# Kernel tuning notes

Hardware: AMD Instinct MI355X
Metric: run time of the kernel (lower is better)

The kernel has to match this reference:

```python
import jax, jax.numpy as jnp
import numpy as np

PS, R, FS, SS = 3, 2, 3, 10.0
PAD = (PS - 1) // 2  # 1


def extract_patches(x, ps, stride):
    # x: (C, Hp, Wp) already padded -> (C, ps, ps, ho, wo)
    C, Hp, Wp = x.shape
    ho = (Hp - ps) // stride + 1
    wo = (Wp - ps) // stride + 1
    rows = []
    for i in range(ps):
        cols = []
        for j in range(ps):
            cols.append(x[:, i:i + stride * ho:stride, j:j + stride * wo:stride])
        rows.append(jnp.stack(cols, axis=1))
    return jnp.stack(rows, axis=1)


def fuse_diag(S):
    # conv2d of (L,L) 'image' with eye(3) kernel, zero pad 1:
    # out[u,v] = S[u-1,v-1] + S[u,v] + S[u+1,v+1]
    Sp = jnp.pad(S, 1)
    return Sp[:-2, :-2] + Sp[1:-1, 1:-1] + Sp[2:, 2:]


def ca_single(f, b, mask):
    # f, b: (c, h, w); mask: (1, h, w)
    c, h, w = f.shape
    # full-res background patches (replicate pad, stride R) -> reconstruction bank
    b_pad = jnp.pad(b, ((0, 0), (PAD, PAD), (PAD, PAD)), mode='edge')
    bg = extract_patches(b_pad, PS, R)                 # (c,ps,ps,hr,wr)
    hr, wr = bg.shape[3], bg.shape[4]
    L = hr * wr
    bg = bg.reshape(c, PS, PS, L).transpose(3, 0, 1, 2)  # (L,c,ps,ps)
    # nearest 1/R downsample (F.interpolate nearest == strided pick)
    fl = f[:, ::R, ::R]
    bl = b[:, ::R, ::R]
    ml = mask[:, ::R, ::R]
    # shrunk background patches (replicate pad, stride 1) -> matching bank
    bl_pad = jnp.pad(bl, ((0, 0), (PAD, PAD), (PAD, PAD)), mode='edge')
    bgs = extract_patches(bl_pad, PS, 1).reshape(c, PS, PS, L).transpose(3, 0, 1, 2)
    # mask patches (zero pad), valid iff patch mean == 0
    mp = extract_patches(jnp.pad(ml, ((0, 0), (PAD, PAD), (PAD, PAD))), PS, 1)
    mi = (mp.mean(axis=(1, 2)).reshape(L) == 0.0).astype(f.dtype)  # (L,)
    # L2-normalize matching patches (clamped at 1e-4)
    bnorm = jnp.maximum(jnp.sqrt((bgs ** 2).sum(axis=(1, 2, 3))), 1e-4)
    bgs_n = bgs / bnorm[:, None, None, None]
    # score = conv2d(f, patches) with zero pad 1 -> cosine-like correlation
    fp = extract_patches(jnp.pad(fl, ((0, 0), (PAD, PAD), (PAD, PAD))), PS, 1)
    score = jnp.einsum('cijhw,lcij->lhw', fp, bgs_n)   # (L,hr,wr)
    # two-pass diagonal 'fuse' trick
    S = fuse_diag(score.reshape(L, L))
    S = S.reshape(hr, wr, hr, wr).transpose(1, 0, 3, 2).reshape(L, L)
    S = fuse_diag(S)
    score = S.reshape(wr, hr, wr, hr).transpose(1, 0, 3, 2).reshape(L, hr, wr)
    # masked softmax over the L patch axis
    score = score * mi[:, None, None]
    score = jax.nn.softmax(score * SS, axis=0) * mi[:, None, None]
    # conv_transpose2d(score, bg, stride=R, padding=PAD) / 4
    # == conv of R-dilated score with flipped kernel, pad = PS-1-PAD
    w_flip = bg[:, :, ::-1, ::-1].transpose(1, 0, 2, 3)  # (c,L,ps,ps)
    out = jax.lax.conv_general_dilated(
        score[None], w_flip, window_strides=(1, 1),
        padding=[(PS - 1 - PAD, PS - 1 - PAD)] * 2, lhs_dilation=(R, R),
        dimension_numbers=('NCHW', 'OIHW', 'NCHW'))[0] / 4.0  # (c,2hr-1,2wr-1)
    if out.shape[1] % 2 == 1:  # static shape check, matches torch branch
        out = jnp.pad(out, ((0, 0), (0, 1), (0, 1)), mode='edge')
    return out


def setup_inputs() -> dict:
    key = jax.random.key(0)
    k1, k2, k3 = jax.random.split(key, 3)
    B, c, h, w = 4, 128, 128, 128
    f = jax.random.normal(k1, (B, c, h, w), dtype=jnp.float32)
    b = jax.random.normal(k2, (B, c, h, w), dtype=jnp.float32)
    mask = jax.random.bernoulli(k3, 0.25, (B, 1, h, w)).astype(jnp.float32)
    return {'f': f, 'b': b, 'mask': mask}


def reference(f, b, mask):
    return jax.vmap(ca_single)(f, b, mask)
```

## Files before the change

### kernel.cpp

```cpp
#include <hip/hip_runtime.h>
#include <cstdint>

#define LVAL 4096
#define K1 1152
#define NT1 18
#define CCH 128
#define HH 128
#define WW 128
#define SSCALE 10.0f
#define NUPAD 2048
#define NACTPAD 512
#define PADPIX 4356
#define PIMG 557568

typedef __attribute__((ext_vector_type(8))) short short8;
typedef __attribute__((ext_vector_type(8))) _Float16 half8;
typedef __attribute__((ext_vector_type(4))) float f32x4;

static __device__ __forceinline__ int clampi(int v, int lo, int hi) {
    return v < lo ? lo : (v > hi ? hi : v);
}
static __device__ __forceinline__ unsigned short f2h(float x) {
    union { _Float16 h; unsigned short u; } c; c.h = (_Float16)x; return c.u;
}
static __device__ __forceinline__ float h2f(unsigned short u) {
    union { _Float16 h; unsigned short u; } c; c.u = u; return (float)c.h;
}

__global__ __launch_bounds__(256) void dst_kernel(const float* __restrict__ f,
        const float* __restrict__ b, unsigned short* __restrict__ fpad4,
        unsigned short* __restrict__ bpad4) {
    __shared__ float t[32][65];
    int h = blockIdx.x;
    int cg = blockIdx.y;
    int za = blockIdx.z;
    int img = za >> 1, arr = za & 1;
    const float* src = (arr ? b : f) + (size_t)img * CCH * HH * WW;
    unsigned short* dst = (arr ? bpad4 : fpad4) + (size_t)img * PIMG;
    int tid = threadIdx.x;
    int w = tid & 63, csub = tid >> 6;
    #pragma unroll
    for (int cc = 0; cc < 8; ++cc) {
        int cl = csub * 8 + cc;
        int ch = cg * 32 + cl;
        t[cl][w] = src[(size_t)ch * (HH * WW) + (2 * h) * WW + (2 * w)];
    }
    __syncthreads();
    int c = tid & 31, pr = tid >> 5;
    #pragma unroll
    for (int pp = 0; pp < 8; ++pp) {
        int w2 = pr * 8 + pp;
        dst[((size_t)(h + 1) * 66 + (w2 + 1)) * 128 + cg * 32 + c] = f2h(t[c][w2]);
    }
}

__global__ __launch_bounds__(256) void qk_border_kernel(unsigned short* __restrict__ fpad4,
        unsigned short* __restrict__ bpad4, float* __restrict__ Q) {
    int img = blockIdx.y;
    int tid = threadIdx.x;
    if (blockIdx.x < 1024) {
        int lane = tid & 63, sub = tid >> 6;
        int pix = blockIdx.x * 4 + sub;
        const unsigned short* row = bpad4 + (size_t)img * PIMG
                                    + ((size_t)((pix >> 6) + 1) * 66 + (pix & 63) + 1) * 128;
        uint32_t hv = *(const uint32_t*)(row + lane * 2);
        float a = h2f((unsigned short)(hv & 0xffff));
        float b2 = h2f((unsigned short)(hv >> 16));
        float s = a * a + b2 * b2;
        for (int off = 32; off > 0; off >>= 1) s += __shfl_xor(s, off, 64);
        if (lane == 0) Q[img * 4096 + pix] = s;
    } else {
        int id = (blockIdx.x - 1024) * 256 + tid;
        if (id >= PADPIX * 16) return;
        int pix = id >> 4, cg = (id & 15) << 3;
        int hp = pix / 66, wp = pix - hp * 66;
        if (hp >= 1 && hp <= 64 && wp >= 1 && wp <= 64) return;
        unsigned short* fp = fpad4 + (size_t)img * PIMG + (size_t)pix * 128 + cg;
        #pragma unroll
        for (int cc = 0; cc < 8; ++cc) fp[cc] = 0;
        int hs = clampi(hp - 1, 0, 63), wsx = clampi(wp - 1, 0, 63);
        const unsigned short* sb = bpad4 + (size_t)img * PIMG
                                   + ((size_t)(hs + 1) * 66 + (wsx + 1)) * 128 + cg;
        unsigned short* bp = bpad4 + (size_t)img * PIMG + (size_t)pix * 128 + cg;
        #pragma unroll
        for (int cc = 0; cc < 8; ++cc) bp[cc] = sb[cc];
    }
}

__global__ __launch_bounds__(1024) void compact_kernel(const float* __restrict__ mask,
        const float* __restrict__ Q, int* __restrict__ act, int* __restrict__ ulist,
        short* __restrict__ tapu, float* __restrict__ invn, int* __restrict__ hdr) {
    int img = blockIdx.x;
    const float* mk = mask + (size_t)img * HH * WW;
    const float* Qi = Q + img * 4096;
    int* acti = act + img * NACTPAD;
    int* uli = ulist + img * NUPAD;
    short* tpi = tapu + (size_t)img * NACTPAD * 12;
    float* invi = invn + (size_t)img * NUPAD;
    int* hd = hdr + img * 4;
    int tid = threadIdx.x;
    int lane = tid & 63, wv = tid >> 6;
    __shared__ unsigned char flag[4096];
    __shared__ short umap[4096];
    __shared__ int actl[NACTPAD];
    __shared__ float ssl[4096];
    __shared__ int wsum[16], woff[16];
    __shared__ int tot;

    int loc[4];
    int cnt = 0;
    #pragma unroll
    for (int k = 0; k < 4; ++k) {
        int a = tid * 4 + k;
        int hb = a >> 6, wb = a & 63;
        float s = 0.f;
        for (int di = -1; di <= 1; ++di)
            for (int dj = -1; dj <= 1; ++dj) {
                int hh = hb + di, w2 = wb + dj;
                if (hh >= 0 && hh < 64 && w2 >= 0 && w2 < 64)
                    s += mk[(2 * hh) * WW + 2 * w2];
            }
        loc[k] = (s == 0.f) ? 1 : 0;
        cnt += loc[k];
    }
    int pre = cnt;
    for (int off = 1; off < 64; off <<= 1) { int v = __shfl_up(pre, off, 64); if (lane >= off) pre += v; }
    if (lane == 63) wsum[wv] = pre;
    __syncthreads();
    if (tid == 0) { int a2 = 0; for (int w2 = 0; w2 < 16; ++w2) { woff[w2] = a2; a2 += wsum[w2]; } tot = a2; }
    __syncthreads();
    int base = woff[wv] + pre - cnt;
    int n_act = tot < NACTPAD ? tot : NACTPAD;
    {
        int p = base;
        #pragma unroll
        for (int k = 0; k < 4; ++k)
            if (loc[k]) { if (p < NACTPAD) { acti[p] = tid * 4 + k; actl[p] = tid * 4 + k; } p++; }
    }
    #pragma unroll
    for (int k = 0; k < 4; ++k) { flag[tid * 4 + k] = 0; umap[tid * 4 + k] = -1; }
    __syncthreads();
    for (int j = tid; j < n_act; j += 1024) {
        int a = actl[j];
        int sa = ((a & 63) << 6) + (a >> 6);
        #pragma unroll
        for (int ei = 0; ei < 3; ++ei) {
            int tbt = sa + ei - 1;
            if (tbt < 0 || tbt >= 4096) continue;
            int tb = ((tbt & 63) << 6) + (tbt >> 6);
            #pragma unroll
            for (int d = -1; d <= 1; ++d) {
                int rb = tb + d;
                if (rb >= 0 && rb < 4096) flag[rb] = 1;
            }
        }
    }
    __syncthreads();
    int cnt2 = 0;
    int loc2[4];
    #pragma unroll
    for (int k = 0; k < 4; ++k) { loc2[k] = flag[tid * 4 + k]; cnt2 += loc2[k]; }
    int pre2 = cnt2;
    for (int off = 1; off < 64; off <<= 1) { int v = __shfl_up(pre2, off, 64); if (lane >= off) pre2 += v; }
    if (lane == 63) wsum[wv] = pre2;
    __syncthreads();
    if (tid == 0) { int a2 = 0; for (int w2 = 0; w2 < 16; ++w2) { woff[w2] = a2; a2 += wsum[w2]; } tot = a2; }
    __syncthreads();
    int base2 = woff[wv] + pre2 - cnt2;
    int n_u = tot < NUPAD ? tot : NUPAD;
    {
        int p = base2;
        #pragma unroll
        for (int k = 0; k < 4; ++k)
            if (loc2[k]) { int ci = tid * 4 + k; if (p < NUPAD) { uli[p] = ci; umap[ci] = (short)p; } p++; }
    }
    __syncthreads();
    for (int j = tid; j < n_act; j += 1024) {
        int a = actl[j];
        int sa = ((a & 63) << 6) + (a >> 6);
        #pragma unroll
        for (int ei = 0; ei < 3; ++ei) {
            int tbt = sa + ei - 1;
            int ok = (tbt >= 0 && tbt < 4096);
            int tb = ok ? ((tbt & 63) << 6) + (tbt >> 6) : 0;
            #pragma unroll
            for (int d = -1; d <= 1; ++d) {
                short v = -1;
                if (ok) { int rb = tb + d; if (rb >= 0 && rb < 4096) v = umap[rb]; }
                tpi[j * 12 + ei * 3 + d + 1] = v;
            }
        }
    }
    for (int a = tid; a < 4096; a += 1024) {
        int hb = a >> 6, wb = a & 63;
        float s = 0.f;
        #pragma unroll
        for (int i = 0; i < 3; ++i)
            #pragma unroll
            for (int j2 = 0; j2 < 3; ++j2) {
                int hl = clampi(hb + i - 1, 0, 63);
                int wl = clampi(wb + j2 - 1, 0, 63);
                s += Qi[hl * 64 + wl];
            }
        ssl[a] = s;
    }
    for (int u = tid; u < NUPAD; u += 1024) invi[u] = 0.f;
    __syncthreads();
    for (int ci = tid; ci < 4096; ci += 1024) {
        if (flag[ci]) {
            int u = umap[ci];
            if (u >= 0) invi[u] = 1.f / fmaxf(sqrtf(ssl[ci]), 1e-4f);
        }
    }
    if (tid == 0) { hd[0] = n_act; hd[1] = n_u; }
}

__global__ void prep_bgtc_kernel(const float* __restrict__ b, const int* __restrict__ act,
                                 const int* __restrict__ hdr, unsigned short* __restrict__ BGTc4) {
    int gimg = blockIdx.y;
    const float* bi = b + (size_t)gimg * CCH * HH * WW;
    int idx = blockIdx.x * 256 + threadIdx.x;
    int k2 = idx >> 9, j = idx & 511;
    int n_act = hdr[gimg * 4];
    unsigned short v = 0;
    if (j < n_act) {
        int a = act[gimg * NACTPAD + j];
        int ch = k2 & 127, q = k2 >> 7;
        int i = q / 3, jj = q - i * 3;
        int y = clampi(2 * (a >> 6) + i - 1, 0, 127);
        int x = clampi(2 * (a & 63) + jj - 1, 0, 127);
        v = f2h(bi[(size_t)ch * (HH * WW) + y * WW + x]);
    }
    BGTc4[(size_t)gimg * K1 * NACTPAD + idx] = v;
}

#define BAR() __builtin_amdgcn_s_barrier()
#define WAITV6() asm volatile("s_waitcnt vmcnt(6)" ::: "memory")
#define WAITV0() asm volatile("s_waitcnt vmcnt(0)" ::: "memory")

#define STAGEX(tt, h) do {                                                              \
    int t_ = (tt);                                                                      \
    if (t_ < NT1) {                                                                     \
        const int isB_ = ((h) == 1 || (h) == 2);                                        \
        const int hi_ = ((h) >= 2) ? 1 : 0;                                             \
        int q_ = t_ >> 1;                                                               \
        int qi_ = (q_ * 11) >> 5;                                                       \
        int qj_ = q_ - qi_ * 3;                                                         \
        int toff_ = ((qi_ * 66 + qj_) << 7) + ((t_ & 1) << 6);                          \
        _Pragma("unroll")                                                               \
        for (int r_ = 0; r_ < 2; ++r_) {                                                \
            int sl_ = hi_ * 2 + r_;                                                     \
            const unsigned short* g_ = (isB_ ? bR[sl_] : aR[sl_]) + toff_;              \
            unsigned short* l_ = lds + (isB_ ? 32768 : 0) + ((t_ & 1) << 14)            \
                                 + ((hi_ * 128 + r_ * 64 + swb) << 6);                  \
            __builtin_amdgcn_global_load_lds((const uint32_t*)(const void*)g_,          \
                                             (uint32_t*)(void*)l_, 16, 0, 0);           \
        }                                                                               \
    } } while (0)

#define LDA4(dst, cur, ah) do {                                                         \
    _Pragma("unroll")                                                                   \
    for (int f_ = 0; f_ < 4; ++f_)                                                      \
    { _Pragma("unroll")                                                                 \
      for (int s_ = 0; s_ < 2; ++s_) {                                                  \
        int row_ = wm * 128 + ((ah) * 4 + f_) * 16 + row16;                             \
        int cs_ = ((s_ << 2) + kgrp) ^ (row16 & 7);                                     \
        dst[f_ * 2 + s_] = *(const half8*)(lds + ((cur) << 14) + (row_ << 6) + (cs_ << 3)); \
    } } } while (0)

#define LDB2(cur, bh) do {                                                              \
    _Pragma("unroll")                                                                   \
    for (int f_ = 0; f_ < 2; ++f_)                                                      \
    { _Pragma("unroll")                                                                 \
      for (int s_ = 0; s_ < 2; ++s_) {                                                  \
        int row_ = wn * 64 + ((bh) * 2 + f_) * 16 + row16;                              \
        int cs_ = ((s_ << 2) + kgrp) ^ (row16 & 7);                                     \
        bv[(bh) * 4 + f_ * 2 + s_] = *(const half8*)(lds + 32768 + ((cur) << 14) + (row_ << 6) + (cs_ << 3)); \
    } } } while (0)

#define MFMA16(va, ai, bj) do {                                                         \
    __builtin_amdgcn_s_setprio(1);                                                      \
    _Pragma("unroll")                                                                   \
    for (int f_ = 0; f_ < 4; ++f_)                                                      \
    { _Pragma("unroll")                                                                 \
      for (int g_ = 0; g_ < 2; ++g_)                                                    \
      { _Pragma("unroll")                                                               \
        for (int s_ = 0; s_ < 2; ++s_)                                                  \
            acc[(ai) * 4 + f_][(bj) * 2 + g_] = __builtin_amdgcn_mfma_f32_16x16x32_f16( \
                va[f_ * 2 + s_], bv[(bj) * 4 + g_ * 2 + s_], acc[(ai) * 4 + f_][(bj) * 2 + g_], 0, 0, 0); \
    } } __builtin_amdgcn_s_setprio(0); } while (0)

__global__ __launch_bounds__(512, 2) void gemm1_8phase(const unsigned short* __restrict__ fpad4,
        const unsigned short* __restrict__ bpad4, unsigned short* __restrict__ Scc4,
        const int* __restrict__ ulist, const int* __restrict__ hdr,
        const float* __restrict__ invn) {
    __shared__ unsigned short lds[65536];
    const int gimg = blockIdx.y;
    const unsigned short* fpadI = fpad4 + (size_t)gimg * PIMG;
    const unsigned short* bpadI = bpad4 + (size_t)gimg * PIMG;
    unsigned short* C = Scc4 + (size_t)gimg * 4096 * NUPAD;
    const int* uli = ulist + gimg * NUPAD;
    const float* invi = invn + (size_t)gimg * NUPAD;
    const int n_u = hdr[gimg * 4 + 1];
    const int tid = threadIdx.x;
    const int lane = tid & 63;
    const int wave = tid >> 6;
    const int wm = wave >> 2, wn = wave & 3;
    const int row16 = lane & 15, kgrp = lane >> 4;
    const int srow = tid >> 3, schunk = tid & 7;
    const int swb = wave << 3;
    int bid = blockIdx.x;
    int wgid = ((bid & 7) << 4) + (bid >> 3);
    const int bm = (wgid >> 3) << 8;
    const int bn = (wgid & 7) << 8;
    if (bn >= ((n_u + 255) & ~255)) return;

    const int ck8 = (schunk ^ (srow & 7)) << 3;
    const unsigned short* aR[4];
    const unsigned short* bR[4];
    #pragma unroll
    for (int i2 = 0; i2 < 4; ++i2) {
        int rowp = i2 * 64 + srow;
        int ar = bm + rowp;
        aR[i2] = fpadI + (size_t)((ar >> 6) * 66 + (ar & 63)) * 128 + ck8;
        int uu = bn + rowp;
        int brow = uli[uu < n_u ? uu : n_u - 1];
        bR[i2] = bpadI + (size_t)((brow >> 6) * 66 + (brow & 63)) * 128 + ck8;
    }

    f32x4 acc[8][4];
    #pragma unroll
    for (int i = 0; i < 8; ++i)
        #pragma unroll
        for (int j = 0; j < 4; ++j)
            acc[i][j] = (f32x4){0.f, 0.f, 0.f, 0.f};

    STAGEX(0, 1); STAGEX(0, 2); STAGEX(0, 0); STAGEX(0, 3);
    STAGEX(1, 1); STAGEX(1, 2); STAGEX(1, 0);
    WAITV6();
    BAR();

    half8 av0[8], av1[8], bv[8];
    for (int t = 0; t < NT1; ++t) {
        const int cur = t & 1;
        LDA4(av0, cur, 0);
        LDB2(cur, 0);
        LDB2(cur, 1);
        STAGEX(t + 1, 3);
        BAR();
        MFMA16(av0, 0, 0);
        LDA4(av1, cur, 1);
        BAR();
        STAGEX(t + 2, 1);
        BAR();
        MFMA16(av0, 0, 1);
        BAR();
        STAGEX(t + 2, 2);
        BAR();
        MFMA16(av1, 1, 0);
        BAR();
        STAGEX(t + 2, 0);
        BAR();
        MFMA16(av1, 1, 1);
        if (t >= NT1 - 2) { WAITV0(); } else { WAITV6(); }
        BAR();
    }

    float iv[4];
    #pragma unroll
    for (int fj = 0; fj < 4; ++fj)
        iv[fj] = invi[bn + wn * 64 + fj * 16 + row16];
    #pragma unroll
    for (int fi = 0; fi < 8; ++fi) {
        int crow = bm + wm * 128 + fi * 16 + kgrp * 4;
        #pragma unroll
        for (int fj = 0; fj < 4; ++fj) {
            int ccol = bn + wn * 64 + fj * 16 + row16;
            f32x4 v = acc[fi][fj];
            #pragma unroll
            for (int r = 0; r < 4; ++r)
                C[(size_t)(crow + r) * NUPAD + ccol] = f2h(v[r] * iv[fj]);
        }
    }
}

__global__ __launch_bounds__(512) void fuse_softmax_kernel(const unsigned short* __restrict__ Scc4,
        const int* __restrict__ hdr, const short* __restrict__ tapu,
        unsigned short* __restrict__ Pc4) {
    __shared__ unsigned short lrow[3][NUPAD];
    __shared__ float redm[8][8], reds[8][8];
    int gimg = blockIdx.y;
    const unsigned short* Scc = Scc4 + (size_t)gimg * 4096 * NUPAD;
    int bid = blockIdx.x;
    int sb0 = ((bid & 7) << 9) + ((bid >> 3) << 3);
    int tid = threadIdx.x;
    int lane = tid & 63, wv = tid >> 6;
    int n_act = hdr[gimg * 4];
    int n_u = hdr[gimg * 4 + 1];
    int nu_s = (n_u + 15) & ~15;
    if (nu_s > NUPAD) nu_s = NUPAD;
    bool actv = tid < n_act;
    short tp[9];
    if (actv) {
        const short* tpp = tapu + ((size_t)gimg * NACTPAD + tid) * 12;
        #pragma unroll
        for (int t = 0; t < 9; ++t) tp[t] = tpp[t];
    }
    float s[8] = {0.f, 0.f, 0.f, 0.f, 0.f, 0.f, 0.f, 0.f};
    for (int ph = 0; ph < 10; ++ph) {
        int tt = sb0 - 1 + ph;
        int ok = (tt >= 0 && tt < 4096);
        int ta = ok ? ((tt & 63) << 6) + (tt >> 6) : 0;
        int vmask = 0;
        #pragma unroll
        for (int dp = 0; dp < 3; ++dp) {
            int ra = ta + dp - 1;
            if (ok && ra >= 0 && ra < 4096) {
                vmask |= 1 << dp;
                const unsigned short* src = Scc + (size_t)ra * NUPAD;
                for (int u = tid * 8; u < nu_s; u += 4096)
                    *(uint4*)&lrow[dp][u] = *(const uint4*)(src + u);
            }
        }
        __syncthreads();
        if (actv) {
            #pragma unroll
            for (int j = 0; j < 8; ++j) {
                int ei = ph - j;
                if (ei >= 0 && ei < 3) {
                    #pragma unroll
                    for (int dp = 0; dp < 3; ++dp) {
                        if ((vmask >> dp) & 1) {
                            int u = tp[ei * 3 + dp];
                            if (u >= 0) s[j] += h2f(lrow[dp][u]);
                        }
                    }
                }
            }
        }
        __syncthreads();
    }
    float m[8], e[8];
    #pragma unroll
    for (int j = 0; j < 8; ++j) {
        float x = actv ? SSCALE * s[j] : -3.0e38f;
        for (int off = 32; off > 0; off >>= 1) x = fmaxf(x, __shfl_xor(x, off, 64));
        if (lane == 0) redm[wv][j] = x;
    }
    __syncthreads();
    #pragma unroll
    for (int j = 0; j < 8; ++j) {
        float mm = -3.0e38f;
        #pragma unroll
        for (int w2 = 0; w2 < 8; ++w2) mm = fmaxf(mm, redm[w2][j]);
        m[j] = fmaxf(mm, 0.f);
        e[j] = actv ? __expf(SSCALE * s[j] - m[j]) : 0.f;
        float sm = e[j];
        for (int off = 32; off > 0; off >>= 1) sm += __shfl_xor(sm, off, 64);
        if (lane == 0) reds[wv][j] = sm;
    }
    __syncthreads();
    #pragma unroll
    for (int j = 0; j < 8; ++j) {
        float S = 0.f;
        #pragma unroll
        for (int w2 = 0; w2 < 8; ++w2) S += reds[w2][j];
        float denom = S + (4096.f - (float)n_act) * __expf(-m[j]);
        int sbj = sb0 + j;
        int b = ((sbj & 63) << 6) + (sbj >> 6);
        Pc4[(size_t)gimg * 4096 * NACTPAD + (size_t)b * NACTPAD + tid] = f2h(actv ? e[j] / denom : 0.f);
    }
}

#define G2STAGE(bs, kk) do {                                                            \
    _Pragma("unroll")                                                                   \
    for (int r_ = 0; r_ < 4; ++r_) {                                                    \
        int row_ = (wave << 5) + (r_ << 3) + rsub;                                      \
        const unsigned short* ga_ = A + (size_t)(bm + row_) * NACTPAD + (kk) + gcol;    \
        unsigned short* la_ = lds + (bs) * 16384 + (((wave << 5) + (r_ << 3)) << 6);    \
        __builtin_amdgcn_global_load_lds((const uint32_t*)(const void*)ga_,             \
                                         (uint32_t*)(void*)la_, 16, 0, 0);              \
        const unsigned short* gb_ = B + (size_t)(bn + row_) * NACTPAD + (kk) + gcol;    \
        unsigned short* lb_ = lds + (bs) * 16384 + 8192 + (((wave << 5) + (r_ << 3)) << 6); \
        __builtin_amdgcn_global_load_lds((const uint32_t*)(const void*)gb_,             \
                                         (uint32_t*)(void*)lb_, 16, 0, 0);              \
    } } while (0)

__global__ __launch_bounds__(256) void gemm2_nt(
        const unsigned short* __restrict__ BGTc4, const unsigned short* __restrict__ Pc4,
        const int* __restrict__ hdr, unsigned short* __restrict__ OUTT4) {
    __shared__ unsigned short lds[2 * 16384];
    const int gimg = blockIdx.z;
    const unsigned short* A = BGTc4 + (size_t)gimg * K1 * NACTPAD;
    const unsigned short* B = Pc4 + (size_t)gimg * 4096 * NACTPAD;
    unsigned short* C = OUTT4 + (size_t)gimg * K1 * LVAL;
    int n_act = hdr[gimg * 4];
    int kend = (n_act + 63) & ~63;
    if (kend < 64) kend = 64;
    const int tid = threadIdx.x;
    const int wave = tid >> 6, lane = tid & 63;
    const int wm = wave >> 1, wn = wave & 1;
    const int bm = blockIdx.y << 7, bn = blockIdx.x << 7;
    const int rsub = lane >> 3, csub = lane & 7;
    const int gcol = (csub ^ rsub) << 3;
    const int row16 = lane & 15, kgrp = lane >> 4;
    const int sw = (row16 & 7) << 3;

    f32x4 acc[4][4];
    #pragma unroll
    for (int i = 0; i < 4; ++i)
        #pragma unroll
        for (int j = 0; j < 4; ++j)
            acc[i][j] = (f32x4){0.f, 0.f, 0.f, 0.f};

    G2STAGE(0, 0);
    WAITV0();
    __syncthreads();
    int nt = kend >> 6;
    for (int t = 0; t < nt; ++t) {
        const int cs = t & 1;
        if (t + 1 < nt) G2STAGE(cs ^ 1, (t + 1) << 6);
        const unsigned short* Asm = lds + cs * 16384;
        const unsigned short* Bsm = lds + cs * 16384 + 8192;
        #pragma unroll
        for (int s = 0; s < 2; ++s) {
            half8 af[4], bfr[4];
            #pragma unroll
            for (int fi = 0; fi < 4; ++fi) {
                int ar = (wm << 6) + (fi << 4) + row16;
                af[fi] = *(const half8*)(Asm + (ar << 6) + (((s << 5) + (kgrp << 3)) ^ sw));
            }
            #pragma unroll
            for (int fj = 0; fj < 4; ++fj) {
                int br = (wn << 6) + (fj << 4) + row16;
                bfr[fj] = *(const half8*)(Bsm + (br << 6) + (((s << 5) + (kgrp << 3)) ^ sw));
            }
            #pragma unroll
            for (int fi = 0; fi < 4; ++fi)
                #pragma unroll
                for (int fj = 0; fj < 4; ++fj)
                    acc[fi][fj] = __builtin_amdgcn_mfma_f32_16x16x32_f16(
                        af[fi], bfr[fj], acc[fi][fj], 0, 0, 0);
        }
        WAITV0();
        __syncthreads();
    }
    #pragma unroll
    for (int fi = 0; fi < 4; ++fi) {
        int crow = bm + (wm << 6) + (fi << 4) + (kgrp << 2);
        #pragma unroll
        for (int fj = 0; fj < 4; ++fj) {
            int ccol = bn + (wn << 6) + (fj << 4) + row16;
            f32x4 v = acc[fi][fj];
            #pragma unroll
            for (int r = 0; r < 4; ++r)
                C[(size_t)(crow + r) * LVAL + ccol] = f2h(v[r]);
        }
    }
}

__global__ void scatter_kernel(const unsigned short* __restrict__ OUTT4,
                               float* __restrict__ out) {
    int gimg = blockIdx.y;
    const unsigned short* OUTT = OUTT4 + (size_t)gimg * K1 * LVAL;
    float* oi = out + (size_t)gimg * CCH * HH * WW;
    int idx = blockIdx.x * 256 + threadIdx.x;
    int x = idx & 127;
    int y = (idx >> 7) & 127;
    int ch = idx >> 14;
    int yy = y < 127 ? y : 126;
    int xx = x < 127 ? x : 126;
    int hy[2], iy[2], ny;
    if (yy & 1) { hy[0] = (yy + 1) >> 1; iy[0] = 0; hy[1] = (yy - 1) >> 1; iy[1] = 2; ny = 2; }
    else        { hy[0] = yy >> 1;       iy[0] = 1; ny = 1; }
    int wx[2], jx[2], nx;
    if (xx & 1) { wx[0] = (xx + 1) >> 1; jx[0] = 0; wx[1] = (xx - 1) >> 1; jx[1] = 2; nx = 2; }
    else        { wx[0] = xx >> 1;       jx[0] = 1; nx = 1; }
    float s = 0.f;
    for (int u = 0; u < ny; ++u)
        for (int v = 0; v < nx; ++v) {
            int k2 = (iy[u] * 3 + jx[v]) * 128 + ch;
            s += h2f(OUTT[(size_t)k2 * LVAL + (hy[u] << 6) + wx[v]]);
        }
    oi[idx] = s * 0.25f;
}

extern "C" void kernel_launch(void* const* d_in, const int* in_sizes, int n_in,
                              void* d_out, int out_size, void* d_ws, size_t ws_size,
                              hipStream_t stream) {
    const float* f = (const float*)d_in[0];
    const float* b = (const float*)d_in[1];
    const float* mask = (const float*)d_in[2];
    float* out = (float*)d_out;
    char* ws = (char*)d_ws;

    const size_t oQ    = 0;
    const size_t oACT  = 65536;
    const size_t oUL   = 73728;
    const size_t oTAP  = 106496;
    const size_t oHDR  = 155648;
    const size_t oINVN = 156672;
    const size_t oBGTC = 189440;
    const size_t oPC   = 4908032;
    const size_t oFPAD = 21685248;
    const size_t oBPAD = 26145792;
    const size_t oSCC  = 30606336;

    float* Q   = (float*)(ws + oQ);
    int*   ACT = (int*)(ws + oACT);
    int*   UL  = (int*)(ws + oUL);
    short* TAP = (short*)(ws + oTAP);
    int*   HDR = (int*)(ws + oHDR);
    float* INVN = (float*)(ws + oINVN);
    unsigned short* BGTc4 = (unsigned short*)(ws + oBGTC);
    unsigned short* Pc4   = (unsigned short*)(ws + oPC);
    unsigned short* fpad4 = (unsigned short*)(ws + oFPAD);
    unsigned short* bpad4 = (unsigned short*)(ws + oBPAD);
    unsigned short* Scc4 = (unsigned short*)(ws + oSCC);
    unsigned short* OUTT4 = (unsigned short*)(ws + oSCC);

    dst_kernel<<<dim3(64, 4, 8), 256, 0, stream>>>(f, b, fpad4, bpad4);
    qk_border_kernel<<<dim3(1297, 4), 256, 0, stream>>>(fpad4, bpad4, Q);
    compact_kernel<<<4, 1024, 0, stream>>>(mask, Q, ACT, UL, TAP, INVN, HDR);
    prep_bgtc_kernel<<<dim3(2304, 4), 256, 0, stream>>>(b, ACT, HDR, BGTc4);

    gemm1_8phase<<<dim3(128, 4), 512, 0, stream>>>(fpad4, bpad4, Scc4, UL, HDR, INVN);
    fuse_softmax_kernel<<<dim3(512, 4), 512, 0, stream>>>(Scc4, HDR, TAP, Pc4);

    gemm2_nt<<<dim3(32, 9, 4), 256, 0, stream>>>(BGTc4, Pc4, HDR, OUTT4);
    scatter_kernel<<<dim3(8192, 4), 256, 0, stream>>>(OUTT4, out);
    (void)in_sizes; (void)n_in; (void)out_size; (void)ws_size;
}
```

Baseline: 218.7 us.

## Halve GEMM1 K-tile to 32 and simplify pipeline schedule to cut LDS

The first score GEMM now stages 32-wide K slices instead of 64-wide ones, doubling the loop trip count to 36. LDS per block drops from 128KB to 64KB, and the 8-phase interleaved load/MFMA schedule becomes a simpler two-half schedule with loads prefetched two tiles ahead. The LDS swizzle is adapted to the 32-column rows. The aim is to let two 512-thread blocks share a CU and to cut barrier overhead per tile, at the cost of more loop iterations and less overlap within each tile.

```diff
diff --git a/kernel.cpp b/kernel.cpp
--- a/kernel.cpp
+++ b/kernel.cpp
@@ -3,7 +3,7 @@
 
 #define LVAL 4096
 #define K1 1152
-#define NT1 18
+#define NT32 36
 #define CCH 128
 #define HH 128
 #define WW 128
@@ -235,66 +235,56 @@
 }
 
 #define BAR() __builtin_amdgcn_s_barrier()
-#define WAITV6() asm volatile("s_waitcnt vmcnt(6)" ::: "memory")
+#define WAITV4() asm volatile("s_waitcnt vmcnt(4)" ::: "memory")
 #define WAITV0() asm volatile("s_waitcnt vmcnt(0)" ::: "memory")
 
-#define STAGEX(tt, h) do {                                                              \
+#define STAGE32(tt, isB) do {                                                           \
     int t_ = (tt);                                                                      \
-    if (t_ < NT1) {                                                                     \
-        const int isB_ = ((h) == 1 || (h) == 2);                                        \
-        const int hi_ = ((h) >= 2) ? 1 : 0;                                             \
-        int q_ = t_ >> 1;                                                               \
+    if (t_ < NT32) {                                                                    \
+        int q_ = t_ >> 2;                                                               \
         int qi_ = (q_ * 11) >> 5;                                                       \
         int qj_ = q_ - qi_ * 3;                                                         \
-        int toff_ = ((qi_ * 66 + qj_) << 7) + ((t_ & 1) << 6);                          \
+        int toff_ = ((qi_ * 66 + qj_) << 7) + ((t_ & 3) << 5);                          \
+        unsigned short* lb_ = lds + ((isB) ? 16384 : 0) + ((t_ & 1) << 13) + (tid << 3);\
+        const unsigned short* const* rp_ = (isB) ? bR2 : aR2;                           \
         _Pragma("unroll")                                                               \
-        for (int r_ = 0; r_ < 2; ++r_) {                                                \
-            int sl_ = hi_ * 2 + r_;                                                     \
-            const unsigned short* g_ = (isB_ ? bR[sl_] : aR[sl_]) + toff_;              \
-            unsigned short* l_ = lds + (isB_ ? 32768 : 0) + ((t_ & 1) << 14)            \
-                                 + ((hi_ * 128 + r_ * 64 + swb) << 6);                  \
-            __builtin_amdgcn_global_load_lds((const uint32_t*)(const void*)g_,          \
-                                             (uint32_t*)(void*)l_, 16, 0, 0);           \
+        for (int g_ = 0; g_ < 2; ++g_) {                                                \
+            __builtin_amdgcn_global_load_lds((const uint32_t*)(const void*)(rp_[g_] + toff_), \
+                                             (uint32_t*)(void*)(lb_ + (g_ << 12)), 16, 0, 0); \
         }                                                                               \
     } } while (0)
 
-#define LDA4(dst, cur, ah) do {                                                         \
+#define LDA32x(dst, cur, half) do {                                                     \
     _Pragma("unroll")                                                                   \
-    for (int f_ = 0; f_ < 4; ++f_)                                                      \
-    { _Pragma("unroll")                                                                 \
-      for (int s_ = 0; s_ < 2; ++s_) {                                                  \
-        int row_ = wm * 128 + ((ah) * 4 + f_) * 16 + row16;                             \
-        int cs_ = ((s_ << 2) + kgrp) ^ (row16 & 7);                                     \
-        dst[f_ * 2 + s_] = *(const half8*)(lds + ((cur) << 14) + (row_ << 6) + (cs_ << 3)); \
-    } } } while (0)
-
-#define LDB2(cur, bh) do {                                                              \
+    for (int f_ = 0; f_ < 4; ++f_) {                                                    \
+        int row_ = wm * 128 + ((half) * 4 + f_) * 16 + row16;                           \
+        int c_ = kgrp ^ ((row_ >> 1) & 3);                                              \
+        dst[f_] = *(const half8*)(lds + ((cur) << 13) + (row_ << 5) + (c_ << 3));       \
+    } } while (0)
+
+#define LDB32x(cur) do {                                                                \
     _Pragma("unroll")                                                                   \
-    for (int f_ = 0; f_ < 2; ++f_)                                                      \
-    { _Pragma("unroll")                                                                 \
-      for (int s_ = 0; s_ < 2; ++s_) {                                                  \
-        int row_ = wn * 64 + ((bh) * 2 + f_) * 16 + row16;                              \
-        int cs_ = ((s_ << 2) + kgrp) ^ (row16 & 7);                                     \
-        bv[(bh) * 4 + f_ * 2 + s_] = *(const half8*)(lds + 32768 + ((cur) << 14) + (row_ << 6) + (cs_ << 3)); \
-    } } } while (0)
-
-#define MFMA16(va, ai, bj) do {                                                         \
+    for (int g_ = 0; g_ < 4; ++g_) {                                                    \
+        int row_ = wn * 64 + g_ * 16 + row16;                                           \
+        int c_ = kgrp ^ ((row_ >> 1) & 3);                                              \
+        bv[g_] = *(const half8*)(lds + 16384 + ((cur) << 13) + (row_ << 5) + (c_ << 3));\
+    } } while (0)
+
+#define MFMA16x(va, half) do {                                                          \
     __builtin_amdgcn_s_setprio(1);                                                      \
     _Pragma("unroll")                                                                   \
     for (int f_ = 0; f_ < 4; ++f_)                                                      \
     { _Pragma("unroll")                                                                 \
-      for (int g_ = 0; g_ < 2; ++g_)                                                    \
-      { _Pragma("unroll")                                                               \
-        for (int s_ = 0; s_ < 2; ++s_)                                                  \
-            acc[(ai) * 4 + f_][(bj) * 2 + g_] = __builtin_amdgcn_mfma_f32_16x16x32_f16( \
-                va[f_ * 2 + s_], bv[(bj) * 4 + g_ * 2 + s_], acc[(ai) * 4 + f_][(bj) * 2 + g_], 0, 0, 0); \
-    } } __builtin_amdgcn_s_setprio(0); } while (0)
+      for (int g_ = 0; g_ < 4; ++g_)                                                    \
+        acc[(half) * 4 + f_][g_] = __builtin_amdgcn_mfma_f32_16x16x32_f16(              \
+            va[f_], bv[g_], acc[(half) * 4 + f_][g_], 0, 0, 0);                         \
+    } __builtin_amdgcn_s_setprio(0); } while (0)
 
 __global__ __launch_bounds__(512, 2) void gemm1_8phase(const unsigned short* __restrict__ fpad4,
         const unsigned short* __restrict__ bpad4, unsigned short* __restrict__ Scc4,
         const int* __restrict__ ulist, const int* __restrict__ hdr,
         const float* __restrict__ invn) {
-    __shared__ unsigned short lds[65536];
+    __shared__ unsigned short lds[32768];
     const int gimg = blockIdx.y;
     const unsigned short* fpadI = fpad4 + (size_t)gimg * PIMG;
     const unsigned short* bpadI = bpad4 + (size_t)gimg * PIMG;
@@ -307,25 +297,23 @@
     const int wave = tid >> 6;
     const int wm = wave >> 2, wn = wave & 3;
     const int row16 = lane & 15, kgrp = lane >> 4;
-    const int srow = tid >> 3, schunk = tid & 7;
-    const int swb = wave << 3;
     int bid = blockIdx.x;
     int wgid = ((bid & 7) << 4) + (bid >> 3);
     const int bm = (wgid >> 3) << 8;
     const int bn = (wgid & 7) << 8;
     if (bn >= ((n_u + 255) & ~255)) return;
 
-    const int ck8 = (schunk ^ (srow & 7)) << 3;
-    const unsigned short* aR[4];
-    const unsigned short* bR[4];
-    #pragma unroll
-    for (int i2 = 0; i2 < 4; ++i2) {
-        int rowp = i2 * 64 + srow;
-        int ar = bm + rowp;
-        aR[i2] = fpadI + (size_t)((ar >> 6) * 66 + (ar & 63)) * 128 + ck8;
-        int uu = bn + rowp;
+    const int srow4 = tid >> 2;
+    const int ckn = (((tid & 3) ^ ((tid >> 3) & 3)) << 3);
+    const unsigned short* aR2[2];
+    const unsigned short* bR2[2];
+    #pragma unroll
+    for (int g2 = 0; g2 < 2; ++g2) {
+        int ar = bm + g2 * 128 + srow4;
+        aR2[g2] = fpadI + (size_t)((ar >> 6) * 66 + (ar & 63)) * 128 + ckn;
+        int uu = bn + g2 * 128 + srow4;
         int brow = uli[uu < n_u ? uu : n_u - 1];
-        bR[i2] = bpadI + (size_t)((brow >> 6) * 66 + (brow & 63)) * 128 + ck8;
+        bR2[g2] = bpadI + (size_t)((brow >> 6) * 66 + (brow & 63)) * 128 + ckn;
     }
 
     f32x4 acc[8][4];
@@ -335,34 +323,24 @@
         for (int j = 0; j < 4; ++j)
             acc[i][j] = (f32x4){0.f, 0.f, 0.f, 0.f};
 
-    STAGEX(0, 1); STAGEX(0, 2); STAGEX(0, 0); STAGEX(0, 3);
-    STAGEX(1, 1); STAGEX(1, 2); STAGEX(1, 0);
-    WAITV6();
+    STAGE32(0, 0); STAGE32(0, 1); STAGE32(1, 0); STAGE32(1, 1);
+    WAITV4();
     BAR();
 
-    half8 av0[8], av1[8], bv[8];
-    for (int t = 0; t < NT1; ++t) {
+    half8 av[4], av2[4], bv[4];
+    for (int t = 0; t < NT32; ++t) {
         const int cur = t & 1;
-        LDA4(av0, cur, 0);
-        LDB2(cur, 0);
-        LDB2(cur, 1);
-        STAGEX(t + 1, 3);
+        LDA32x(av, cur, 0);
+        LDB32x(cur);
         BAR();
-        MFMA16(av0, 0, 0);
-        LDA4(av1, cur, 1);
+        MFMA16x(av, 0);
         BAR();
-        STAGEX(t + 2, 1);
+        LDA32x(av2, cur, 1);
         BAR();
-        MFMA16(av0, 0, 1);
-        BAR();
-        STAGEX(t + 2, 2);
-        BAR();
-        MFMA16(av1, 1, 0);
-        BAR();
-        STAGEX(t + 2, 0);
-        BAR();
-        MFMA16(av1, 1, 1);
-        if (t >= NT1 - 2) { WAITV0(); } else { WAITV6(); }
+        MFMA16x(av2, 1);
+        STAGE32(t + 2, 0);
+        STAGE32(t + 2, 1);
+        if (t >= NT32 - 2) { WAITV0(); } else { WAITV4(); }
         BAR();
     }
 
```

Result: no change. 221.2 us (+1.1%).

## Shrink gemm1 block tile from 256x256 to 128x256 and restructure pipeline

Applied to the files above, without the earlier changes.

The first GEMM's tile changes from 256x256 to 128x256 (M halved), so twice as many workgroups launch (256 per image) and each wave accumulates 4x4 fragments instead of 8x4. LDS use falls to 96KB per block and the staging and MFMA schedule is rebuilt into two phases per K step with new load groupings and a new vmcnt wait count. The aim is more parallelism and less register and LDS pressure, so occupancy rises and the tail shrinks on a GPU with many CUs. The cost is lower arithmetic intensity per tile and more redundant B loads.

```diff
diff --git a/kernel.cpp b/kernel.cpp
--- a/kernel.cpp
+++ b/kernel.cpp
@@ -235,50 +235,60 @@
 }
 
 #define BAR() __builtin_amdgcn_s_barrier()
-#define WAITV6() asm volatile("s_waitcnt vmcnt(6)" ::: "memory")
+#define WAITV4() asm volatile("s_waitcnt vmcnt(4)" ::: "memory")
 #define WAITV0() asm volatile("s_waitcnt vmcnt(0)" ::: "memory")
 
-#define STAGEX(tt, h) do {                                                              \
-    int t_ = (tt);                                                                      \
-    if (t_ < NT1) {                                                                     \
-        const int isB_ = ((h) == 1 || (h) == 2);                                        \
-        const int hi_ = ((h) >= 2) ? 1 : 0;                                             \
-        int q_ = t_ >> 1;                                                               \
-        int qi_ = (q_ * 11) >> 5;                                                       \
-        int qj_ = q_ - qi_ * 3;                                                         \
-        int toff_ = ((qi_ * 66 + qj_) << 7) + ((t_ & 1) << 6);                          \
-        _Pragma("unroll")                                                               \
-        for (int r_ = 0; r_ < 2; ++r_) {                                                \
-            int sl_ = hi_ * 2 + r_;                                                     \
-            const unsigned short* g_ = (isB_ ? bR[sl_] : aR[sl_]) + toff_;              \
-            unsigned short* l_ = lds + (isB_ ? 32768 : 0) + ((t_ & 1) << 14)            \
-                                 + ((hi_ * 128 + r_ * 64 + swb) << 6);                  \
-            __builtin_amdgcn_global_load_lds((const uint32_t*)(const void*)g_,          \
-                                             (uint32_t*)(void*)l_, 16, 0, 0);           \
-        }                                                                               \
+#define STAGE_A(tt) do { int t_ = (tt); if (t_ < NT1) {                                 \
+    int q_ = t_ >> 1; int qi_ = (q_ * 11) >> 5; int qj_ = q_ - qi_ * 3;                 \
+    int toff_ = ((qi_ * 66 + qj_) << 7) + ((t_ & 1) << 6);                              \
+    unsigned short* l_ = lds + (t_ & 1) * 24576 + (tid << 3);                           \
+    _Pragma("unroll")                                                                   \
+    for (int g_ = 0; g_ < 2; ++g_)                                                      \
+        __builtin_amdgcn_global_load_lds((const uint32_t*)(const void*)(aR2[g_] + toff_), \
+                                         (uint32_t*)(void*)(l_ + g_ * 4096), 16, 0, 0); \
     } } while (0)
 
-#define LDA4(dst, cur, ah) do {                                                         \
+#define STAGE_BLO(tt) do { int t_ = (tt); if (t_ < NT1) {                               \
+    int q_ = t_ >> 1; int qi_ = (q_ * 11) >> 5; int qj_ = q_ - qi_ * 3;                 \
+    int toff_ = ((qi_ * 66 + qj_) << 7) + ((t_ & 1) << 6);                              \
+    unsigned short* l_ = lds + (t_ & 1) * 24576 + 8192 + (tid << 3);                    \
+    _Pragma("unroll")                                                                   \
+    for (int g_ = 0; g_ < 2; ++g_)                                                      \
+        __builtin_amdgcn_global_load_lds((const uint32_t*)(const void*)(bR2[g_] + toff_), \
+                                         (uint32_t*)(void*)(l_ + g_ * 4096), 16, 0, 0); \
+    } } while (0)
+
+#define STAGE_BHI(tt) do { int t_ = (tt); if (t_ < NT1) {                               \
+    int q_ = t_ >> 1; int qi_ = (q_ * 11) >> 5; int qj_ = q_ - qi_ * 3;                 \
+    int toff_ = ((qi_ * 66 + qj_) << 7) + ((t_ & 1) << 6);                              \
+    unsigned short* l_ = lds + (t_ & 1) * 24576 + 8192 + (tid << 3);                    \
+    _Pragma("unroll")                                                                   \
+    for (int g_ = 2; g_ < 4; ++g_)                                                      \
+        __builtin_amdgcn_global_load_lds((const uint32_t*)(const void*)(bR2[g_] + toff_), \
+                                         (uint32_t*)(void*)(l_ + g_ * 4096), 16, 0, 0); \
+    } } while (0)
+
+#define LDA8(cur) do {                                                                  \
     _Pragma("unroll")                                                                   \
     for (int f_ = 0; f_ < 4; ++f_)                                                      \
     { _Pragma("unroll")                                                                 \
       for (int s_ = 0; s_ < 2; ++s_) {                                                  \
-        int row_ = wm * 128 + ((ah) * 4 + f_) * 16 + row16;                             \
+        int row_ = wm * 64 + f_ * 16 + row16;                                           \
         int cs_ = ((s_ << 2) + kgrp) ^ (row16 & 7);                                     \
-        dst[f_ * 2 + s_] = *(const half8*)(lds + ((cur) << 14) + (row_ << 6) + (cs_ << 3)); \
+        av[f_ * 2 + s_] = *(const half8*)(lds + (cur) * 24576 + (row_ << 6) + (cs_ << 3)); \
     } } } while (0)
 
-#define LDB2(cur, bh) do {                                                              \
+#define LDBH(dst, cur, bh) do {                                                         \
     _Pragma("unroll")                                                                   \
     for (int f_ = 0; f_ < 2; ++f_)                                                      \
     { _Pragma("unroll")                                                                 \
       for (int s_ = 0; s_ < 2; ++s_) {                                                  \
         int row_ = wn * 64 + ((bh) * 2 + f_) * 16 + row16;                              \
         int cs_ = ((s_ << 2) + kgrp) ^ (row16 & 7);                                     \
-        bv[(bh) * 4 + f_ * 2 + s_] = *(const half8*)(lds + 32768 + ((cur) << 14) + (row_ << 6) + (cs_ << 3)); \
+        dst[f_ * 2 + s_] = *(const half8*)(lds + (cur) * 24576 + 8192 + (row_ << 6) + (cs_ << 3)); \
     } } } while (0)
 
-#define MFMA16(va, ai, bj) do {                                                         \
+#define MFMAC(bvx, bj) do {                                                             \
     __builtin_amdgcn_s_setprio(1);                                                      \
     _Pragma("unroll")                                                                   \
     for (int f_ = 0; f_ < 4; ++f_)                                                      \
@@ -286,15 +296,15 @@
       for (int g_ = 0; g_ < 2; ++g_)                                                    \
       { _Pragma("unroll")                                                               \
         for (int s_ = 0; s_ < 2; ++s_)                                                  \
-            acc[(ai) * 4 + f_][(bj) * 2 + g_] = __builtin_amdgcn_mfma_f32_16x16x32_f16( \
-                va[f_ * 2 + s_], bv[(bj) * 4 + g_ * 2 + s_], acc[(ai) * 4 + f_][(bj) * 2 + g_], 0, 0, 0); \
+            acc[f_][(bj) * 2 + g_] = __builtin_amdgcn_mfma_f32_16x16x32_f16(            \
+                av[f_ * 2 + s_], bvx[g_ * 2 + s_], acc[f_][(bj) * 2 + g_], 0, 0, 0);    \
     } } __builtin_amdgcn_s_setprio(0); } while (0)
 
 __global__ __launch_bounds__(512, 2) void gemm1_8phase(const unsigned short* __restrict__ fpad4,
         const unsigned short* __restrict__ bpad4, unsigned short* __restrict__ Scc4,
         const int* __restrict__ ulist, const int* __restrict__ hdr,
         const float* __restrict__ invn) {
-    __shared__ unsigned short lds[65536];
+    __shared__ unsigned short lds[49152];
     const int gimg = blockIdx.y;
     const unsigned short* fpadI = fpad4 + (size_t)gimg * PIMG;
     const unsigned short* bpadI = bpad4 + (size_t)gimg * PIMG;
@@ -307,62 +317,55 @@
     const int wave = tid >> 6;
     const int wm = wave >> 2, wn = wave & 3;
     const int row16 = lane & 15, kgrp = lane >> 4;
-    const int srow = tid >> 3, schunk = tid & 7;
-    const int swb = wave << 3;
     int bid = blockIdx.x;
-    int wgid = ((bid & 7) << 4) + (bid >> 3);
-    const int bm = (wgid >> 3) << 8;
+    int wgid = ((bid & 7) << 5) + (bid >> 3);
+    const int bm = (wgid >> 3) << 7;
     const int bn = (wgid & 7) << 8;
     if (bn >= ((n_u + 255) & ~255)) return;
 
+    const int srow = tid >> 3, schunk = tid & 7;
     const int ck8 = (schunk ^ (srow & 7)) << 3;
-    const unsigned short* aR[4];
-    const unsigned short* bR[4];
-    #pragma unroll
-    for (int i2 = 0; i2 < 4; ++i2) {
-        int rowp = i2 * 64 + srow;
-        int ar = bm + rowp;
-        aR[i2] = fpadI + (size_t)((ar >> 6) * 66 + (ar & 63)) * 128 + ck8;
-        int uu = bn + rowp;
+    const unsigned short* aR2[2];
+    const unsigned short* bR2[4];
+    #pragma unroll
+    for (int g2 = 0; g2 < 2; ++g2) {
+        int ar = bm + g2 * 64 + srow;
+        aR2[g2] = fpadI + (size_t)((ar >> 6) * 66 + (ar & 63)) * 128 + ck8;
+    }
+    #pragma unroll
+    for (int g2 = 0; g2 < 4; ++g2) {
+        int uu = bn + g2 * 64 + srow;
         int brow = uli[uu < n_u ? uu : n_u - 1];
-        bR[i2] = bpadI + (size_t)((brow >> 6) * 66 + (brow & 63)) * 128 + ck8;
-    }
-
-    f32x4 acc[8][4];
-    #pragma unroll
-    for (int i = 0; i < 8; ++i)
+        bR2[g2] = bpadI + (size_t)((brow >> 6) * 66 + (brow & 63)) * 128 + ck8;
+    }
+
+    f32x4 acc[4][4];
+    #pragma unroll
+    for (int i = 0; i < 4; ++i)
         #pragma unroll
         for (int j = 0; j < 4; ++j)
             acc[i][j] = (f32x4){0.f, 0.f, 0.f, 0.f};
 
-    STAGEX(0, 1); STAGEX(0, 2); STAGEX(0, 0); STAGEX(0, 3);
-    STAGEX(1, 1); STAGEX(1, 2); STAGEX(1, 0);
-    WAITV6();
+    STAGE_A(0); STAGE_BLO(0); STAGE_BHI(0);
+    STAGE_A(1); STAGE_BLO(1);
+    WAITV4();
     BAR();
 
-    half8 av0[8], av1[8], bv[8];
+    half8 av[8], bvlo[4], bvhi[4];
     for (int t = 0; t < NT1; ++t) {
         const int cur = t & 1;
-        LDA4(av0, cur, 0);
-        LDB2(cur, 0);
-        LDB2(cur, 1);
-        STAGEX(t + 1, 3);
+        LDA8(cur);
+        LDBH(bvlo, cur, 0);
+        STAGE_BHI(t + 1);
         BAR();
-        MFMA16(av0, 0, 0);
-        LDA4(av1, cur, 1);
+        MFMAC(bvlo, 0);
         BAR();
-        STAGEX(t + 2, 1);
+        LDBH(bvhi, cur, 1);
+        STAGE_A(t + 2);
+        STAGE_BLO(t + 2);
         BAR();
-        MFMA16(av0, 0, 1);
-        BAR();
-        STAGEX(t + 2, 2);
-        BAR();
-        MFMA16(av1, 1, 0);
-        BAR();
-        STAGEX(t + 2, 0);
-        BAR();
-        MFMA16(av1, 1, 1);
-        if (t >= NT1 - 2) { WAITV0(); } else { WAITV6(); }
+        MFMAC(bvhi, 1);
+        if (t >= NT1 - 2) { WAITV0(); } else { WAITV4(); }
         BAR();
     }
 
@@ -371,8 +374,8 @@
     for (int fj = 0; fj < 4; ++fj)
         iv[fj] = invi[bn + wn * 64 + fj * 16 + row16];
     #pragma unroll
-    for (int fi = 0; fi < 8; ++fi) {
-        int crow = bm + wm * 128 + fi * 16 + kgrp * 4;
+    for (int fi = 0; fi < 4; ++fi) {
+        int crow = bm + wm * 64 + fi * 16 + kgrp * 4;
         #pragma unroll
         for (int fj = 0; fj < 4; ++fj) {
             int ccol = bn + wn * 64 + fj * 16 + row16;
@@ -624,7 +627,7 @@
     compact_kernel<<<4, 1024, 0, stream>>>(mask, Q, ACT, UL, TAP, INVN, HDR);
     prep_bgtc_kernel<<<dim3(2304, 4), 256, 0, stream>>>(b, ACT, HDR, BGTc4);
 
-    gemm1_8phase<<<dim3(128, 4), 512, 0, stream>>>(fpad4, bpad4, Scc4, UL, HDR, INVN);
+    gemm1_8phase<<<dim3(256, 4), 512, 0, stream>>>(fpad4, bpad4, Scc4, UL, HDR, INVN);
     fuse_softmax_kernel<<<dim3(512, 4), 512, 0, stream>>>(Scc4, HDR, TAP, Pc4);
 
     gemm2_nt<<<dim3(32, 9, 4), 256, 0, stream>>>(BGTc4, Pc4, HDR, OUTT4);
```

Measured after the change: 232.3 us. 6.2% more time.

## Widen gemm2 tile to 128x256 with 8 waves and split B fragment loads

Applied to the files above, without the earlier changes.

The second GEMM now uses 512-thread blocks, each computing a 128x256 output tile instead of 128x128, which halves the grid along N and reuses each A tile across twice as many columns. Global-to-LDS staging uses precomputed per-thread row pointers. The B fragments are loaded in two halves, each followed by its own MFMA batch under raised wave priority, so LDS reads overlap with matrix math. In exchange, each block uses more LDS and registers, and the grid has fewer blocks, which may reduce occupancy and leave more of the GPU idle.

```diff
diff --git a/kernel.cpp b/kernel.cpp
--- a/kernel.cpp
+++ b/kernel.cpp
@@ -472,24 +472,60 @@
     }
 }
 
-#define G2STAGE(bs, kk) do {                                                            \
-    _Pragma("unroll")                                                                   \
-    for (int r_ = 0; r_ < 4; ++r_) {                                                    \
-        int row_ = (wave << 5) + (r_ << 3) + rsub;                                      \
-        const unsigned short* ga_ = A + (size_t)(bm + row_) * NACTPAD + (kk) + gcol;    \
-        unsigned short* la_ = lds + (bs) * 16384 + (((wave << 5) + (r_ << 3)) << 6);    \
-        __builtin_amdgcn_global_load_lds((const uint32_t*)(const void*)ga_,             \
-                                         (uint32_t*)(void*)la_, 16, 0, 0);              \
-        const unsigned short* gb_ = B + (size_t)(bn + row_) * NACTPAD + (kk) + gcol;    \
-        unsigned short* lb_ = lds + (bs) * 16384 + 8192 + (((wave << 5) + (r_ << 3)) << 6); \
-        __builtin_amdgcn_global_load_lds((const uint32_t*)(const void*)gb_,             \
-                                         (uint32_t*)(void*)lb_, 16, 0, 0);              \
+#define G2SA(tt) do { int t_ = (tt); if (t_ < nt) {                                     \
+    int ko_ = t_ << 6;                                                                  \
+    unsigned short* l_ = lds + (t_ & 1) * 24576 + (tid << 3);                           \
+    _Pragma("unroll")                                                                   \
+    for (int g_ = 0; g_ < 2; ++g_)                                                      \
+        __builtin_amdgcn_global_load_lds((const uint32_t*)(const void*)(aP[g_] + ko_),  \
+                                         (uint32_t*)(void*)(l_ + g_ * 4096), 16, 0, 0); \
     } } while (0)
 
-__global__ __launch_bounds__(256) void gemm2_nt(
+#define G2SB(tt) do { int t_ = (tt); if (t_ < nt) {                                     \
+    int ko_ = t_ << 6;                                                                  \
+    unsigned short* l_ = lds + (t_ & 1) * 24576 + 8192 + (tid << 3);                    \
+    _Pragma("unroll")                                                                   \
+    for (int g_ = 0; g_ < 4; ++g_)                                                      \
+        __builtin_amdgcn_global_load_lds((const uint32_t*)(const void*)(bP[g_] + ko_),  \
+                                         (uint32_t*)(void*)(l_ + g_ * 4096), 16, 0, 0); \
+    } } while (0)
+
+#define G2LDA(cur) do {                                                                 \
+    _Pragma("unroll")                                                                   \
+    for (int f_ = 0; f_ < 4; ++f_)                                                      \
+    { _Pragma("unroll")                                                                 \
+      for (int s_ = 0; s_ < 2; ++s_) {                                                  \
+        int row_ = wm * 64 + f_ * 16 + row16;                                           \
+        int cs_ = ((s_ << 2) + kgrp) ^ (row16 & 7);                                     \
+        av[f_ * 2 + s_] = *(const half8*)(lds + (cur) * 24576 + (row_ << 6) + (cs_ << 3)); \
+    } } } while (0)
+
+#define G2LDB(dst, cur, bh) do {                                                        \
+    _Pragma("unroll")                                                                   \
+    for (int f_ = 0; f_ < 2; ++f_)                                                      \
+    { _Pragma("unroll")                                                                 \
+      for (int s_ = 0; s_ < 2; ++s_) {                                                  \
+        int row_ = wn * 64 + ((bh) * 2 + f_) * 16 + row16;                              \
+        int cs_ = ((s_ << 2) + kgrp) ^ (row16 & 7);                                     \
+        dst[f_ * 2 + s_] = *(const half8*)(lds + (cur) * 24576 + 8192 + (row_ << 6) + (cs_ << 3)); \
+    } } } while (0)
+
+#define G2MFMA(bvx, bj) do {                                                            \
+    __builtin_amdgcn_s_setprio(1);                                                      \
+    _Pragma("unroll")                                                                   \
+    for (int f_ = 0; f_ < 4; ++f_)                                                      \
+    { _Pragma("unroll")                                                                 \
+      for (int g_ = 0; g_ < 2; ++g_)                                                    \
+      { _Pragma("unroll")                                                               \
+        for (int s_ = 0; s_ < 2; ++s_)                                                  \
+            acc[f_][(bj) * 2 + g_] = __builtin_amdgcn_mfma_f32_16x16x32_f16(            \
+                av[f_ * 2 + s_], bvx[f_ * 0 + g_ * 2 + s_], acc[f_][(bj) * 2 + g_], 0, 0, 0); \
+    } } __builtin_amdgcn_s_setprio(0); } while (0)
+
+__global__ __launch_bounds__(512) void gemm2_nt(
         const unsigned short* __restrict__ BGTc4, const unsigned short* __restrict__ Pc4,
         const int* __restrict__ hdr, unsigned short* __restrict__ OUTT4) {
-    __shared__ unsigned short lds[2 * 16384];
+    __shared__ unsigned short lds[49152];
     const int gimg = blockIdx.z;
     const unsigned short* A = BGTc4 + (size_t)gimg * K1 * NACTPAD;
     const unsigned short* B = Pc4 + (size_t)gimg * 4096 * NACTPAD;
@@ -497,14 +533,25 @@
     int n_act = hdr[gimg * 4];
     int kend = (n_act + 63) & ~63;
     if (kend < 64) kend = 64;
+    const int nt = kend >> 6;
     const int tid = threadIdx.x;
-    const int wave = tid >> 6, lane = tid & 63;
-    const int wm = wave >> 1, wn = wave & 1;
-    const int bm = blockIdx.y << 7, bn = blockIdx.x << 7;
-    const int rsub = lane >> 3, csub = lane & 7;
-    const int gcol = (csub ^ rsub) << 3;
+    const int lane = tid & 63;
+    const int wave = tid >> 6;
+    const int wm = wave >> 2, wn = wave & 3;
     const int row16 = lane & 15, kgrp = lane >> 4;
-    const int sw = (row16 & 7) << 3;
+    const int bm = blockIdx.y << 7;
+    const int bn = blockIdx.x << 8;
+
+    const int srow = tid >> 3;
+    const int ck8 = (((tid & 7) ^ (srow & 7)) << 3);
+    const unsigned short* aP[2];
+    const unsigned short* bP[4];
+    #pragma unroll
+    for (int g2 = 0; g2 < 2; ++g2)
+        aP[g2] = A + (size_t)(bm + g2 * 64 + srow) * NACTPAD + ck8;
+    #pragma unroll
+    for (int g2 = 0; g2 < 4; ++g2)
+        bP[g2] = B + (size_t)(bn + g2 * 64 + srow) * NACTPAD + ck8;
 
     f32x4 acc[4][4];
     #pragma unroll
@@ -513,44 +560,28 @@
         for (int j = 0; j < 4; ++j)
             acc[i][j] = (f32x4){0.f, 0.f, 0.f, 0.f};
 
-    G2STAGE(0, 0);
+    G2SA(0); G2SB(0);
     WAITV0();
     __syncthreads();
-    int nt = kend >> 6;
+
+    half8 av[8], bvlo[4], bvhi[4];
     for (int t = 0; t < nt; ++t) {
-        const int cs = t & 1;
-        if (t + 1 < nt) G2STAGE(cs ^ 1, (t + 1) << 6);
-        const unsigned short* Asm = lds + cs * 16384;
-        const unsigned short* Bsm = lds + cs * 16384 + 8192;
-        #pragma unroll
-        for (int s = 0; s < 2; ++s) {
-            half8 af[4], bfr[4];
-            #pragma unroll
-            for (int fi = 0; fi < 4; ++fi) {
-                int ar = (wm << 6) + (fi << 4) + row16;
-                af[fi] = *(const half8*)(Asm + (ar << 6) + (((s << 5) + (kgrp << 3)) ^ sw));
-            }
-            #pragma unroll
-            for (int fj = 0; fj < 4; ++fj) {
-                int br = (wn << 6) + (fj << 4) + row16;
-                bfr[fj] = *(const half8*)(Bsm + (br << 6) + (((s << 5) + (kgrp << 3)) ^ sw));
-            }
-            #pragma unroll
-            for (int fi = 0; fi < 4; ++fi)
-                #pragma unroll
-                for (int fj = 0; fj < 4; ++fj)
-                    acc[fi][fj] = __builtin_amdgcn_mfma_f32_16x16x32_f16(
-                        af[fi], bfr[fj], acc[fi][fj], 0, 0, 0);
-        }
+        const int cur = t & 1;
+        G2SA(t + 1); G2SB(t + 1);
+        G2LDA(cur);
+        G2LDB(bvlo, cur, 0);
+        G2MFMA(bvlo, 0);
+        G2LDB(bvhi, cur, 1);
+        G2MFMA(bvhi, 1);
         WAITV0();
         __syncthreads();
     }
     #pragma unroll
     for (int fi = 0; fi < 4; ++fi) {
-        int crow = bm + (wm << 6) + (fi << 4) + (kgrp << 2);
+        int crow = bm + wm * 64 + fi * 16 + kgrp * 4;
         #pragma unroll
         for (int fj = 0; fj < 4; ++fj) {
-            int ccol = bn + (wn << 6) + (fj << 4) + row16;
+            int ccol = bn + wn * 64 + fj * 16 + row16;
             f32x4 v = acc[fi][fj];
             #pragma unroll
             for (int r = 0; r < 4; ++r)
@@ -627,7 +658,7 @@
     gemm1_8phase<<<dim3(128, 4), 512, 0, stream>>>(fpad4, bpad4, Scc4, UL, HDR, INVN);
     fuse_softmax_kernel<<<dim3(512, 4), 512, 0, stream>>>(Scc4, HDR, TAP, Pc4);
 
-    gemm2_nt<<<dim3(32, 9, 4), 256, 0, stream>>>(BGTc4, Pc4, HDR, OUTT4);
+    gemm2_nt<<<dim3(16, 9, 4), 512, 0, stream>>>(BGTc4, Pc4, HDR, OUTT4);
     scatter_kernel<<<dim3(8192, 4), 256, 0, stream>>>(OUTT4, out);
     (void)in_sizes; (void)n_in; (void)out_size; (void)ws_size;
 }
```

After: 221.2 us. No clear change (+1.1%).
